# Kernel optimization log

Hardware: AMD Instinct MI355X
Metric: run time of the kernel (lower is better)

The kernel has to match this reference:

```python
import jax, jax.numpy as jnp
import numpy as np

HEADS = 8
RADIUS = 50
EPS = 1e-5


def conv1d(x, w, b, stride, pad):
    # x: [B, Cin, T], w: [Cout, Cin, K] (torch OIH layout)
    y = jax.lax.conv_general_dilated(x, w, (stride,), [(pad, pad)],
                                     dimension_numbers=("NCH", "OIH", "NCH"))
    return y + b[None, :, None]


def mm1x1(x, w, b):
    # pointwise Conv1d: w [Cout, Cin]
    return jnp.einsum("oc,bct->bot", w, x) + b[None, :, None]


def lstm_layer(xT, Wih, Whh, bih, bhh):
    # xT: [T, B, Cin]; torch gate order i, f, g, o
    B = xT.shape[1]
    Hh = Whh.shape[1]
    h0 = jnp.zeros((B, Hh), xT.dtype)

    def step(carry, xt):
        h, c = carry
        g = xt @ Wih.T + h @ Whh.T + bih + bhh
        i, f, gg, o = jnp.split(g, 4, axis=-1)
        c = jax.nn.sigmoid(f) * c + jax.nn.sigmoid(i) * jnp.tanh(gg)
        h = jax.nn.sigmoid(o) * jnp.tanh(c)
        return (h, c), h

    _, ys = jax.lax.scan(step, (h0, h0), xT)
    return ys


def attention(x, q_w, q_b, k_w, k_b, c_w, c_b, rel_emb, fc_w, fc_b, bn_g, bn_b, attn_scale):
    B, C, L = x.shape
    D = C // HEADS
    split = lambda y: y.reshape(B, HEADS, D, L)
    q = split(mm1x1(x, q_w, q_b))
    k = split(mm1x1(x, k_w, k_b))
    cnt = split(mm1x1(x, c_w, c_b))
    dots = jnp.einsum("bhct,bhcs->bhts", q, k)  # no 1/sqrt(d): faithful to source
    steps = jnp.arange(L)
    rel = steps[:, None] - steps[None, :]                       # [L, L]
    embs = rel_emb[RADIUS + jnp.clip(rel, -RADIUS, RADIUS)]     # [L, L, D]
    dots = dots + 0.3 * jnp.einsum("bhct,tsc->bhts", q, embs)
    dots = jnp.where((jnp.abs(rel) <= RADIUS)[None, None], dots, -jnp.inf)
    w = jax.nn.softmax(dots, axis=-1)
    out = jnp.einsum("bhts,bhcs->bhct", w, cnt) + 0.3 * jnp.einsum("bhts,tsc->bhct", w, embs)
    out = out.reshape(B, C, L)
    out = mm1x1(out, fc_w, fc_b)
    # BatchNorm1d, training-mode statistics over (batch, time)
    mu = out.mean(axis=(0, 2), keepdims=True)
    var = ((out - mu) ** 2).mean(axis=(0, 2), keepdims=True)
    out = (out - mu) * jax.lax.rsqrt(var + EPS) * bn_g[None, :, None] + bn_b[None, :, None]
    return jax.nn.relu(out) * attn_scale[None, :, None]


def forward(meg, conv1_w, conv1_b, conv2_w, conv2_b, subj_emb,
            W_ih0, W_hh0, b_ih0, b_hh0, W_ih1, W_hh1, b_ih1, b_hh1,
            q_w, q_b, k_w, k_b, c_w, c_b, rel_emb, fc_w, fc_b, bn_g, bn_b,
            attn_scale, out_w, out_b, subjects):
    # ConvSequence encoder: two strided convs, LeakyReLU(0.0) == ReLU
    x = jax.nn.relu(conv1d(meg, conv1_w, conv1_b, 2, 2))
    x = jax.nn.relu(conv1d(x, conv2_w, conv2_b, 2, 2))          # [B, 512, L]
    B, _, L = x.shape
    emb = subj_emb[subjects]                                    # ScaledEmbedding, scale=1.0
    x = jnp.concatenate([x, jnp.broadcast_to(emb[:, :, None], (B, emb.shape[1], L))], axis=1)
    xT = x.transpose(2, 0, 1)                                   # [L, B, 576]
    xT = lstm_layer(xT, W_ih0, W_hh0, b_ih0, b_hh0)
    xT = lstm_layer(xT, W_ih1, W_hh1, b_ih1, b_hh1)
    x = xT.transpose(1, 2, 0)                                   # [B, 512, L]
    x = x + attention(x, q_w, q_b, k_w, k_b, c_w, c_b, rel_emb, fc_w, fc_b, bn_g, bn_b, attn_scale)
    return mm1x1(x, out_w, out_b)                               # [B, 128, L]


def setup_inputs() -> dict:
    key = jax.random.key(0)
    ks = iter(jax.random.split(key, 40))
    nk = lambda: next(ks)
    r = lambda shape, s=0.05: jax.random.normal(nk(), shape, jnp.float32) * s
    # relative-position embedding with the cumsum/sqrt init from the source
    rel = jax.random.normal(nk(), (2 * RADIUS + 1, 64), jnp.float32) * 0.05
    rel = jnp.cumsum(rel, axis=0) / jnp.sqrt(jnp.arange(1, 2 * RADIUS + 2, dtype=jnp.float32))[:, None]
    return dict(
        meg=jax.random.normal(nk(), (8, 273, 2048), jnp.float32),
        conv1_w=r((512, 273, 4)), conv1_b=r((512,)),
        conv2_w=r((512, 512, 4)), conv2_b=r((512,)),
        subj_emb=r((200, 64), 0.1),
        W_ih0=r((2048, 576)), W_hh0=r((2048, 512)), b_ih0=r((2048,)), b_hh0=r((2048,)),
        W_ih1=r((2048, 512)), W_hh1=r((2048, 512)), b_ih1=r((2048,)), b_hh1=r((2048,)),
        q_w=r((512, 512)), q_b=r((512,)),
        k_w=r((512, 512)), k_b=r((512,)),
        c_w=r((512, 512)), c_b=r((512,)),
        rel_emb=rel,
        fc_w=r((512, 512)), fc_b=r((512,)),
        bn_g=jnp.ones((512,), jnp.float32), bn_b=jnp.zeros((512,), jnp.float32),
        attn_scale=jnp.full((512,), 0.1, jnp.float32),
        out_w=r((128, 512)), out_b=r((128,)),
        subjects=jax.random.randint(nk(), (8,), 0, 200),
    )


def reference(meg, conv1_w, conv1_b, conv2_w, conv2_b, subj_emb,
              W_ih0, W_hh0, b_ih0, b_hh0, W_ih1, W_hh1, b_ih1, b_hh1,
              q_w, q_b, k_w, k_b, c_w, c_b, rel_emb, fc_w, fc_b, bn_g, bn_b,
              attn_scale, out_w, out_b, subjects):
    return forward(meg, conv1_w, conv1_b, conv2_w, conv2_b, subj_emb,
                   W_ih0, W_hh0, b_ih0, b_hh0, W_ih1, W_hh1, b_ih1, b_hh1,
                   q_w, q_b, k_w, k_b, c_w, c_b, rel_emb, fc_w, fc_b, bn_g, bn_b,
                   attn_scale, out_w, out_b, subjects)
```

## Files before the change

### kernel.cpp

```cpp
#include <hip/hip_runtime.h>
#include <cstdint>
#include <cmath>

typedef unsigned short u16;
typedef unsigned int u32;
typedef __attribute__((ext_vector_type(8))) short bf16x8;
typedef __attribute__((ext_vector_type(4))) float f32x4;

#define B_    8
#define T_IN  2048
#define CIN1  273
#define L1_   1025
#define L_    513
#define C_    512
#define CE_   576
#define M1_   (B_*L1_)
#define M_    (B_*L_)
#define K1_   (CIN1*4)
#define H_    8
#define D_    64
#define R_    50

__device__ __forceinline__ u32 f2bf_rne(float f) {
    u32 x = __float_as_uint(f);
    return (x + 0x7fffu + ((x >> 16) & 1u)) >> 16;
}

__device__ __forceinline__ u32 a_pair(const void* A, int m, int k, int lda, int amode, int Ksz) {
    if (amode == 2) {
        if (k >= K1_) return 0;
        int b = m / L1_, t = m - b * L1_;
        int ci = k >> 2, kk = k & 3;
        int it = 2 * t - 2 + kk;
        const float* mg = (const float*)A + ((size_t)(b * CIN1 + ci)) * T_IN;
        u32 lo = ((unsigned)it < (unsigned)T_IN)       ? f2bf_rne(mg[it])     : 0;
        u32 hi = ((unsigned)(it + 1) < (unsigned)T_IN) ? f2bf_rne(mg[it + 1]) : 0;
        return lo | (hi << 16);
    } else if (amode == 5) {
        int b = m / L_, t = m - b * L_;
        int kk = k >> 9, ci = k & 511;
        int it = 2 * t - 2 + kk;
        if ((unsigned)it >= (unsigned)L1_) return 0;
        return *(const u32*)((const u16*)A + ((size_t)(b * L1_ + it)) * 512 + ci);
    } else {
        return *(const u32*)((const u16*)A + (size_t)m * lda + k);
    }
}

__global__ __launch_bounds__(256) void gemm_kernel(
    const void* __restrict__ Aptr, const u32* __restrict__ Bp,
    const float* __restrict__ bias1, const float* __restrict__ bias2,
    float* __restrict__ Cf, u16* __restrict__ Cb,
    int Msz, int Nsz, int Ksz, int lda, int ldc, int amode, int cmode, int relu)
{
    __shared__ u16 As[64][40];
    __shared__ u16 Bs[64][40];

    int tid = threadIdx.x;
    int m0 = blockIdx.x * 64, n0 = blockIdx.y * 64;
    int wv = tid >> 6, lane = tid & 63;
    int lm = lane & 15, quad = lane >> 4;
    int kp = tid & 15, rw = tid >> 4;
    int Kh = Ksz >> 1;

    f32x4 acc[4];
#pragma unroll
    for (int nt = 0; nt < 4; ++nt)
#pragma unroll
        for (int r = 0; r < 4; ++r) acc[nt][r] = 0.f;

    for (int k0 = 0; k0 < Ksz; k0 += 32) {
        int pidx = (k0 >> 1) + kp;
#pragma unroll
        for (int i = 0; i < 4; ++i) {
            int row = rw + 16 * i;
            int k = k0 + 2 * kp;
            int m = m0 + row;
            u32 aw = 0;
            if (m < Msz && k < Ksz) aw = a_pair(Aptr, m, k, lda, amode, Ksz);
            *(u32*)&As[row][2 * kp] = aw;
            u32 bw = 0;
            if (pidx < Kh) bw = Bp[(size_t)(n0 + row) * Kh + pidx];
            *(u32*)&Bs[row][2 * kp] = bw;
        }
        __syncthreads();

        bf16x8 af = *(const bf16x8*)&As[wv * 16 + lm][quad * 8];
#pragma unroll
        for (int nt = 0; nt < 4; ++nt) {
            bf16x8 bf = *(const bf16x8*)&Bs[nt * 16 + lm][quad * 8];
            acc[nt] = __builtin_amdgcn_mfma_f32_16x16x32_bf16(af, bf, acc[nt], 0, 0, 0);
        }
        __syncthreads();
    }

#pragma unroll
    for (int nt = 0; nt < 4; ++nt) {
#pragma unroll
        for (int r = 0; r < 4; ++r) {
            int m = m0 + wv * 16 + quad * 4 + r;
            if (m >= Msz) continue;
            int n = n0 + nt * 16 + lm;
            float v = acc[nt][r] + bias1[n] + (bias2 ? bias2[n] : 0.f);
            if (relu) v = fmaxf(v, 0.f);
            if (cmode == 0) {
                Cf[(size_t)m * ldc + n] = v;
            } else if (cmode == 1) {
                int b = m / L_, t = m - b * L_;
                Cf[((size_t)(b * 128 + n)) * L_ + t] = v;
            } else if (cmode == 2) {
                int b = m / L_, t = m - b * L_;
                Cf[((size_t)(t * 8 + b)) * ldc + n] = v;
            } else {
                Cb[(size_t)m * ldc + n] = (u16)f2bf_rne(v);
            }
        }
    }
}

__global__ __launch_bounds__(256) void gemm_qkv(
    const u16* __restrict__ h1b,
    const u32* __restrict__ qwp, const u32* __restrict__ kwp, const u32* __restrict__ cwp,
    const float* __restrict__ qb, const float* __restrict__ kb, const float* __restrict__ cb,
    float* __restrict__ qo, float* __restrict__ ko, float* __restrict__ co)
{
    __shared__ u16 As[64][40];
    __shared__ u16 Bs[64][40];

    int tid = threadIdx.x;
    int which = blockIdx.y >> 3;
    int m0 = blockIdx.x * 64, n0 = (blockIdx.y & 7) * 64;
    const u32* Bp = which == 0 ? qwp : (which == 1 ? kwp : cwp);
    const float* bias = which == 0 ? qb : (which == 1 ? kb : cb);
    float* Cf = which == 0 ? qo : (which == 1 ? ko : co);

    int wv = tid >> 6, lane = tid & 63;
    int lm = lane & 15, quad = lane >> 4;
    int kp = tid & 15, rw = tid >> 4;

    f32x4 acc[4];
#pragma unroll
    for (int nt = 0; nt < 4; ++nt)
#pragma unroll
        for (int r = 0; r < 4; ++r) acc[nt][r] = 0.f;

    for (int k0 = 0; k0 < 512; k0 += 32) {
#pragma unroll
        for (int i = 0; i < 4; ++i) {
            int row = rw + 16 * i;
            int k = k0 + 2 * kp;
            int m = m0 + row;
            u32 aw = 0;
            if (m < M_) {
                int b = m / L_, t = m - b * L_;
                aw = *(const u32*)(h1b + ((size_t)(t * 8 + b)) * 512 + k);
            }
            *(u32*)&As[row][2 * kp] = aw;
            *(u32*)&Bs[row][2 * kp] = Bp[(size_t)(n0 + row) * 256 + (k0 >> 1) + kp];
        }
        __syncthreads();

        bf16x8 af = *(const bf16x8*)&As[wv * 16 + lm][quad * 8];
#pragma unroll
        for (int nt = 0; nt < 4; ++nt) {
            bf16x8 bf = *(const bf16x8*)&Bs[nt * 16 + lm][quad * 8];
            acc[nt] = __builtin_amdgcn_mfma_f32_16x16x32_bf16(af, bf, acc[nt], 0, 0, 0);
        }
        __syncthreads();
    }

#pragma unroll
    for (int nt = 0; nt < 4; ++nt) {
#pragma unroll
        for (int r = 0; r < 4; ++r) {
            int m = m0 + wv * 16 + quad * 4 + r;
            if (m >= M_) continue;
            int n = n0 + nt * 16 + lm;
            Cf[(size_t)m * 512 + n] = acc[nt][r] + bias[n];
        }
    }
}

__global__ __launch_bounds__(256) void emb_kernel(const float* __restrict__ semb,
                                                  const int* __restrict__ subj,
                                                  u16* __restrict__ x2b)
{
    int idx = blockIdx.x * 256 + threadIdx.x;
    if (idx >= M_ * 64) return;
    int m = idx >> 6, e = idx & 63;
    int b = m / L_;
    x2b[(size_t)m * CE_ + 512 + e] = (u16)f2bf_rne(semb[subj[b] * 64 + e]);
}

__global__ __launch_bounds__(256) void pack_b(const float* __restrict__ W, u32* __restrict__ P,
                                              int N, int K)
{
    int gid = blockIdx.x * 256 + threadIdx.x;
    int Kh = K >> 1;
    if (gid >= N * Kh) return;
    int n = gid / Kh, p = gid - n * Kh;
    int k = 2 * p;
    u32 lo = f2bf_rne(W[(size_t)n * K + k]);
    u32 hi = f2bf_rne(W[(size_t)n * K + k + 1]);
    P[gid] = lo | (hi << 16);
}

__global__ __launch_bounds__(256) void pack_post(const float* __restrict__ qw,
                                                 const float* __restrict__ kw,
                                                 const float* __restrict__ cw,
                                                 const float* __restrict__ fcw,
                                                 const float* __restrict__ outw,
                                                 u32* __restrict__ P)
{
    int gid = blockIdx.x * 256 + threadIdx.x;
    if (gid >= 557056) return;
    const float* W;
    int local;
    if (gid < 524288) {
        int wsel = gid >> 17;
        W = wsel == 0 ? qw : (wsel == 1 ? kw : (wsel == 2 ? cw : fcw));
        local = gid & 131071;
    } else {
        W = outw;
        local = gid - 524288;
    }
    int n = local >> 8, p = local & 255;
    int k = 2 * p;
    u32 lo = f2bf_rne(W[(size_t)n * 512 + k]);
    u32 hi = f2bf_rne(W[(size_t)n * 512 + k + 1]);
    P[gid] = lo | (hi << 16);
}

__global__ __launch_bounds__(256) void pack_w2k(const float* __restrict__ W, u32* __restrict__ P)
{
    int gid = blockIdx.x * 256 + threadIdx.x;
    int n = gid >> 10, p = gid & 1023;
    int kk = p >> 8, ci = (2 * p) & 511;
    u32 lo = f2bf_rne(W[(size_t)n * 2048 + ci * 4 + kk]);
    u32 hi = f2bf_rne(W[(size_t)n * 2048 + ci * 4 + 4 + kk]);
    P[gid] = lo | (hi << 16);
}

__global__ __launch_bounds__(256) void pack_w3(const float* __restrict__ W0,
                                               const float* __restrict__ W1,
                                               const float* __restrict__ W2,
                                               u32* __restrict__ P)
{
    int gid3 = blockIdx.x * 256 + threadIdx.x;
    int src = gid3 >> 19;
    int gid = gid3 & 524287;
    const float* W = src == 0 ? W0 : (src == 1 ? W1 : W2);
    int r = gid & 1, lane = (gid >> 1) & 63, i2 = (gid >> 7) & 1;
    int g = (gid >> 8) & 3, j = gid >> 10;
    int row = g * 512 + j;
    int c0 = 4 * (lane + 64 * i2) + 2 * r;
    u32 lo = f2bf_rne(W[(size_t)row * 512 + c0]);
    u32 hi = f2bf_rne(W[(size_t)row * 512 + c0 + 1]);
    P[gid3] = lo | (hi << 16);
}

__global__ __launch_bounds__(256, 1) void lstm_persist(
    const float* __restrict__ pre0,
    const u32* __restrict__ P0,
    const u32* __restrict__ P1,
    const u32* __restrict__ P2,
    const float* __restrict__ bih1,
    const float* __restrict__ bhh1,
    float* __restrict__ h0seq,
    float* __restrict__ h1seq,
    u16* __restrict__ h1b,
    u32* __restrict__ f0,
    u32* __restrict__ f1)
{
    const int layer = blockIdx.x >> 7;
    const int blk = blockIdx.x & 127;
    const int tid = threadIdx.x;
    const int l = tid & 63;
    const int rg = tid >> 6;
    const int j = blk * 4 + rg;

    __shared__ float4 hA4[1024];
    __shared__ float4 hB4[1024];
    __shared__ float part[4 * 8 * 33];
    __shared__ float gates[4 * 33];

    const u32* wA = (layer ? P2 : P0) + (size_t)j * 1024;
    uint2 wra[8], wrb[8];
#pragma unroll
    for (int i2 = 0; i2 < 2; ++i2)
#pragma unroll
        for (int g = 0; g < 4; ++g)
            wra[i2 * 4 + g] = *(const uint2*)&wA[(g * 2 + i2) * 128 + l * 2];
    if (layer) {
        const u32* wB = P1 + (size_t)j * 1024;
#pragma unroll
        for (int i2 = 0; i2 < 2; ++i2)
#pragma unroll
            for (int g = 0; g < 4; ++g)
                wrb[i2 * 4 + g] = *(const uint2*)&wB[(g * 2 + i2) * 128 + l * 2];
    }

    int fb = 0, grow = 0;
    float bias1 = 0.f;
    if (tid < 128) {
        int fw = tid >> 5;
        fb = tid & 7;
        grow = ((tid & 31) >> 3) * 512 + blk * 4 + fw;
        if (layer) bias1 = bih1[grow] + bhh1[grow];
    }

    float creg = 0.f;

    for (int t = 0; t <= L_; ++t) {
        bool active = layer ? (t >= 1) : (t < L_);
        if (!active) continue;
        int tt = layer ? (t - 1) : t;

        float mypre = 0.f;
        if (tid < 128)
            mypre = layer ? bias1 : pre0[((size_t)(tt * 8 + fb)) * 2048 + grow];

        if (tid < 64) {
            const u32* sA = nullptr;
            const u32* sB = nullptr;
            if (layer) {
                sA = f0 + (size_t)tt * 128;
                if (tt > 0) sB = f1 + (size_t)(tt - 1) * 128;
            } else if (tt > 0) {
                sA = f0 + (size_t)(tt - 1) * 128;
            }
            if (sA) {
                bool a0 = false, a1 = false;
                bool b0 = (sB == nullptr), b1 = (sB == nullptr);
                for (;;) {
                    if (!a0) a0 = __hip_atomic_load(&sA[l], __ATOMIC_RELAXED, __HIP_MEMORY_SCOPE_AGENT) != 0u;
                    if (!a1) a1 = __hip_atomic_load(&sA[l + 64], __ATOMIC_RELAXED, __HIP_MEMORY_SCOPE_AGENT) != 0u;
                    if (sB) {
                        if (!b0) b0 = __hip_atomic_load(&sB[l], __ATOMIC_RELAXED, __HIP_MEMORY_SCOPE_AGENT) != 0u;
                        if (!b1) b1 = __hip_atomic_load(&sB[l + 64], __ATOMIC_RELAXED, __HIP_MEMORY_SCOPE_AGENT) != 0u;
                    }
                    if (__all(a0 && a1 && b0 && b1)) break;
                    __builtin_amdgcn_s_sleep(1);
                }
            }
        }
        __syncthreads();

        if (tt == 0) {
#pragma unroll
            for (int i = 0; i < 4; ++i)
                hA4[tid + 256 * i] = make_float4(0.f, 0.f, 0.f, 0.f);
        } else {
            const float4* src = (const float4*)((layer ? h1seq : h0seq) + (size_t)(tt - 1) * 4096);
#pragma unroll
            for (int i = 0; i < 4; ++i)
                hA4[tid + 256 * i] = src[tid + 256 * i];
        }
        if (layer) {
            const float4* src = (const float4*)(h0seq + (size_t)tt * 4096);
#pragma unroll
            for (int i = 0; i < 4; ++i)
                hB4[tid + 256 * i] = src[tid + 256 * i];
        }
        __syncthreads();

        float acc[4][8];
#pragma unroll
        for (int g = 0; g < 4; ++g)
#pragma unroll
            for (int b = 0; b < 8; ++b) acc[g][b] = 0.f;

#pragma unroll
        for (int i2 = 0; i2 < 2; ++i2) {
            int cq = l + 64 * i2;
            float4 hv[8];
#pragma unroll
            for (int b = 0; b < 8; ++b) hv[b] = hA4[b * 128 + cq];
#pragma unroll
            for (int g = 0; g < 4; ++g) {
                uint2 ww = wra[i2 * 4 + g];
                float w0 = __uint_as_float(ww.x << 16);
                float w1 = __uint_as_float(ww.x & 0xffff0000u);
                float w2 = __uint_as_float(ww.y << 16);
                float w3 = __uint_as_float(ww.y & 0xffff0000u);
#pragma unroll
                for (int b = 0; b < 8; ++b)
                    acc[g][b] = fmaf(w0, hv[b].x, fmaf(w1, hv[b].y,
                                fmaf(w2, hv[b].z, fmaf(w3, hv[b].w, acc[g][b]))));
            }
        }
        if (layer) {
#pragma unroll
            for (int i2 = 0; i2 < 2; ++i2) {
                int cq = l + 64 * i2;
                float4 hv[8];
#pragma unroll
                for (int b = 0; b < 8; ++b) hv[b] = hB4[b * 128 + cq];
#pragma unroll
                for (int g = 0; g < 4; ++g) {
                    uint2 ww = wrb[i2 * 4 + g];
                    float w0 = __uint_as_float(ww.x << 16);
                    float w1 = __uint_as_float(ww.x & 0xffff0000u);
                    float w2 = __uint_as_float(ww.y << 16);
                    float w3 = __uint_as_float(ww.y & 0xffff0000u);
#pragma unroll
                    for (int b = 0; b < 8; ++b)
                        acc[g][b] = fmaf(w0, hv[b].x, fmaf(w1, hv[b].y,
                                    fmaf(w2, hv[b].z, fmaf(w3, hv[b].w, acc[g][b]))));
                }
            }
        }

#pragma unroll
        for (int m = 8; m <= 32; m <<= 1)
#pragma unroll
            for (int g = 0; g < 4; ++g)
#pragma unroll
                for (int b = 0; b < 8; ++b)
                    acc[g][b] += __shfl_xor(acc[g][b], m);
        if (l < 8) {
#pragma unroll
            for (int g = 0; g < 4; ++g)
#pragma unroll
                for (int b = 0; b < 8; ++b)
                    part[(rg * 8 + l) * 33 + g * 8 + b] = acc[g][b];
        }
        __syncthreads();

        if (tid < 128) {
            int w = tid >> 5, x = tid & 31;
            float s = 0.f;
#pragma unroll
            for (int p = 0; p < 8; ++p) s += part[(w * 8 + p) * 33 + x];
            gates[w * 33 + x] = s + mypre;
        }
        __syncthreads();

        if (tid < 32) {
            int w = tid >> 3, b = tid & 7;
            float gi = gates[w * 33 + 0 * 8 + b];
            float gf = gates[w * 33 + 1 * 8 + b];
            float gg = gates[w * 33 + 2 * 8 + b];
            float go = gates[w * 33 + 3 * 8 + b];
            int ji = blk * 4 + w;
            float cprev = (tt == 0) ? 0.f : creg;
            float si = 1.f / (1.f + expf(-gi));
            float sf = 1.f / (1.f + expf(-gf));
            float so = 1.f / (1.f + expf(-go));
            float cn = sf * cprev + si * tanhf(gg);
            creg = cn;
            float hv = so * tanhf(cn);
            float* hout = layer ? h1seq : h0seq;
            __hip_atomic_store(&hout[((size_t)tt * 8 + b) * 512 + ji], hv,
                               __ATOMIC_RELAXED, __HIP_MEMORY_SCOPE_AGENT);
            if (layer) h1b[((size_t)tt * 8 + b) * 512 + ji] = (u16)f2bf_rne(hv);
        }
        asm volatile("s_waitcnt vmcnt(0)" ::: "memory");
        if (tid == 0)
            __hip_atomic_store((layer ? f1 : f0) + (size_t)tt * 128 + blk, 1u,
                               __ATOMIC_RELAXED, __HIP_MEMORY_SCOPE_AGENT);
        __syncthreads();
    }
}

__global__ __launch_bounds__(128) void attn_kernel(const float* __restrict__ q,
                                                   const float* __restrict__ k,
                                                   const float* __restrict__ cnt,
                                                   const float* __restrict__ rel,
                                                   u16* __restrict__ outb)
{
    int t = blockIdx.x, h = blockIdx.y, b = blockIdx.z;
    int s_lo = max(0, t - R_), s_hi = min(L_ - 1, t + R_);
    int W = s_hi - s_lo + 1;
    int tid = threadIdx.x;

    __shared__ float qrow[64];
    __shared__ float dots[104];
    __shared__ float red[128];

    const float* qp = q + ((size_t)(b * L_ + t) * C_ + h * D_);
    if (tid < 64) qrow[tid] = qp[tid];
    __syncthreads();

    if (tid < W) {
        int s = s_lo + tid;
        const float* kp = k + ((size_t)(b * L_ + s) * C_ + h * D_);
        const float* rp = rel + (R_ + t - s) * D_;
        float acc = 0.f;
#pragma unroll 8
        for (int d = 0; d < 64; ++d)
            acc += qrow[d] * (kp[d] + 0.3f * rp[d]);
        dots[tid] = acc;
    }
    __syncthreads();

    red[tid] = (tid < W) ? dots[tid] : -INFINITY;
    __syncthreads();
    for (int s = 64; s > 0; s >>= 1) {
        if (tid < s) red[tid] = fmaxf(red[tid], red[tid + s]);
        __syncthreads();
    }
    float mx = red[0];
    __syncthreads();
    float e = 0.f;
    if (tid < W) { e = expf(dots[tid] - mx); dots[tid] = e; }
    red[tid] = e;
    __syncthreads();
    for (int s = 64; s > 0; s >>= 1) {
        if (tid < s) red[tid] += red[tid + s];
        __syncthreads();
    }
    float inv = 1.f / red[0];
    if (tid < W) dots[tid] *= inv;
    __syncthreads();

    if (tid < 64) {
        float acc = 0.f;
        const float* cb = cnt + ((size_t)(b * L_ + s_lo) * C_ + h * D_ + tid);
        const float* rb = rel + (R_ + t - s_lo) * D_ + tid;
        for (int i = 0; i < W; ++i)
            acc += dots[i] * (cb[(size_t)i * C_] + 0.3f * rb[-i * D_]);
        outb[(size_t)(b * L_ + t) * C_ + h * D_ + tid] = (u16)f2bf_rne(acc);
    }
}

__global__ __launch_bounds__(512) void bn_sum(const float* __restrict__ fcout, float* __restrict__ stats)
{
    int c = threadIdx.x;
    float s = 0.f, ss = 0.f;
    for (int m = blockIdx.x; m < M_; m += 32) {
        float v = fcout[(size_t)m * 512 + c];
        s += v; ss += v * v;
    }
    atomicAdd(&stats[c], s);
    atomicAdd(&stats[512 + c], ss);
}

__global__ __launch_bounds__(256) void bn_apply(const float* __restrict__ fcout,
                                                const float* __restrict__ stats,
                                                const float* __restrict__ bng, const float* __restrict__ bnb,
                                                const float* __restrict__ ascl,
                                                const float* __restrict__ h1tm,
                                                u16* __restrict__ xfinb)
{
    int idx = blockIdx.x * 256 + threadIdx.x;
    if (idx >= M_ * 512) return;
    int c = idx & 511;
    int m = idx >> 9;
    int b = m / L_, t = m - b * L_;
    float mean = stats[c] * (1.f / (float)M_);
    float var = stats[512 + c] * (1.f / (float)M_) - mean * mean;
    float rs = rsqrtf(fmaxf(var, 0.f) + 1e-5f);
    float v = (fcout[idx] - mean) * rs * bng[c] + bnb[c];
    v = fmaxf(v, 0.f) * ascl[c];
    xfinb[idx] = (u16)f2bf_rne(h1tm[((size_t)(t * 8 + b)) * 512 + c] + v);
}

extern "C" void kernel_launch(void* const* d_in, const int* in_sizes, int n_in,
                              void* d_out, int out_size, void* d_ws, size_t ws_size,
                              hipStream_t stream)
{
    const float* meg  = (const float*)d_in[0];
    const float* w1   = (const float*)d_in[1];
    const float* b1   = (const float*)d_in[2];
    const float* w2   = (const float*)d_in[3];
    const float* b2   = (const float*)d_in[4];
    const float* semb = (const float*)d_in[5];
    const float* Wih0 = (const float*)d_in[6];
    const float* Whh0 = (const float*)d_in[7];
    const float* bih0 = (const float*)d_in[8];
    const float* bhh0 = (const float*)d_in[9];
    const float* Wih1 = (const float*)d_in[10];
    const float* Whh1 = (const float*)d_in[11];
    const float* bih1 = (const float*)d_in[12];
    const float* bhh1 = (const float*)d_in[13];
    const float* qw   = (const float*)d_in[14];
    const float* qb   = (const float*)d_in[15];
    const float* kw   = (const float*)d_in[16];
    const float* kb   = (const float*)d_in[17];
    const float* cw   = (const float*)d_in[18];
    const float* cbi  = (const float*)d_in[19];
    const float* rel  = (const float*)d_in[20];
    const float* fcw  = (const float*)d_in[21];
    const float* fcb  = (const float*)d_in[22];
    const float* bng  = (const float*)d_in[23];
    const float* bnb  = (const float*)d_in[24];
    const float* ascl = (const float*)d_in[25];
    const float* outw = (const float*)d_in[26];
    const float* outb = (const float*)d_in[27];
    const int* subj = (const int*)d_in[28];
    float* out = (float*)d_out;

    float* ws = (float*)d_ws;
    u16*   x1b   = (u16*)(ws + 0);
    u32*   w1p   = (u32*)(ws + 6562304);
    u32*   w2p   = (u32*)(ws + 6841856);
    u16*   x2b   = (u16*)(ws + 4198400);
    u32*   wih0p = (u32*)(ws + 14967296);
    u32*   P0    = (u32*)(ws + 0);
    u32*   P1    = (u32*)(ws + 524288);
    u32*   P2    = (u32*)(ws + 1048576);
    u32*   flg   = (u32*)(ws + 1572864);
    float* pre0  = ws + 6562304;
    float* h0    = ws + 14967296;
    float* h1    = ws + 17068544;
    u16*   h1b   = (u16*)(ws + 19169792);
    float* qb_f  = ws + 0;
    float* kb_f  = ws + 2101248;
    float* cb_f  = ws + 4202496;
    u16*   attno = (u16*)(ws + 6562304);
    float* fco   = ws + 8663552;
    float* stats = ws + 10764800;
    u32*   qwp   = (u32*)(ws + 10765824);
    u32*   kwp   = (u32*)(ws + 10896896);
    u32*   cwp   = (u32*)(ws + 11027968);
    u32*   fcwp  = (u32*)(ws + 11159040);
    u32*   outwp = (u32*)(ws + 11290112);
    u16*   xfinb = (u16*)(ws + 19169792);

    auto gemm = [&](const void* A, const u32* Bp, const float* bi1, const float* bi2,
                    float* Cf, u16* Cb, int Msz, int Nsz, int Ksz,
                    int lda, int ldc, int amode, int cmode, int relu) {
        dim3 g((Msz + 63) / 64, Nsz / 64);
        gemm_kernel<<<g, 256, 0, stream>>>(A, Bp, bi1, bi2, Cf, Cb,
                                           Msz, Nsz, Ksz, lda, ldc, amode, cmode, relu);
    };

    pack_b<<<(512 * 546 + 255) / 256, 256, 0, stream>>>(w1, w1p, 512, 1092);
    pack_w2k<<<2048, 256, 0, stream>>>(w2, w2p);

    gemm(meg, w1p, b1, nullptr, nullptr, x1b, M1_, 512, K1_, 0, 512, 2, 3, 1);
    gemm(x1b, w2p, b2, nullptr, nullptr, x2b, M_, 512, 2048, 0, CE_, 5, 3, 1);
    emb_kernel<<<(M_ * 64 + 255) / 256, 256, 0, stream>>>(semb, subj, x2b);

    pack_w3<<<6144, 256, 0, stream>>>(Whh0, Wih1, Whh1, P0);
    pack_b<<<(2048 * 288 + 255) / 256, 256, 0, stream>>>(Wih0, wih0p, 2048, 576);

    gemm(x2b, wih0p, bih0, bhh0, pre0, nullptr, M_, 2048, CE_, CE_, 2048, 6, 2, 0);

    hipMemsetAsync(flg, 0, 2 * 514 * 128 * sizeof(u32), stream);
    lstm_persist<<<dim3(256), 256, 0, stream>>>(pre0, P0, P1, P2, bih1, bhh1,
                                                h0, h1, h1b, flg, flg + 514 * 128);

    pack_post<<<(557056 + 255) / 256, 256, 0, stream>>>(qw, kw, cw, fcw, outw, qwp);
    hipMemsetAsync(stats, 0, 1024 * sizeof(float), stream);

    gemm_qkv<<<dim3((M_ + 63) / 64, 24), 256, 0, stream>>>(h1b, qwp, kwp, cwp, qb, kb, cbi,
                                                           qb_f, kb_f, cb_f);

    attn_kernel<<<dim3(L_, H_, B_), 128, 0, stream>>>(qb_f, kb_f, cb_f, rel, attno);

    gemm(attno, fcwp, fcb, nullptr, fco, nullptr, M_, 512, 512, 512, 512, 6, 0, 0);
    bn_sum<<<32, 512, 0, stream>>>(fco, stats);
    bn_apply<<<(M_ * 512 + 255) / 256, 256, 0, stream>>>(fco, stats, bng, bnb, ascl, h1, xfinb);

    gemm(xfinb, outwp, outb, nullptr, out, nullptr, M_, 128, 512, 512, 0, 6, 1, 0);
}
```

Before: 3.691 ms.

## Drop LDS staging of hidden state in persistent LSTM, read h directly per wave

Each wave of the persistent LSTM kernel now polls the cross-block readiness flags itself. It then loads the previous hidden state straight from global memory into registers, instead of one wave polling and the block staging h into shared memory. This removes two block-wide barriers per timestep plus the trailing barrier, and moves the bf16 copy of h1 after the flag publish so it is off the critical path. The latency-bound recurrence should advance faster per step. In exchange each of the four waves re-reads the full hidden vector from L2, and memory ordering now relies more on per-wave flag polling.

```diff
diff --git a/kernel.cpp b/kernel.cpp
--- a/kernel.cpp
+++ b/kernel.cpp
@@ -279,8 +279,6 @@
     const int rg = tid >> 6;
     const int j = blk * 4 + rg;
 
-    __shared__ float4 hA4[1024];
-    __shared__ float4 hB4[1024];
     __shared__ float part[4 * 8 * 33];
     __shared__ float gates[4 * 33];
 
@@ -310,6 +308,7 @@
     }
 
     float creg = 0.f;
+    const float4 z4 = make_float4(0.f, 0.f, 0.f, 0.f);
 
     for (int t = 0; t <= L_; ++t) {
         bool active = layer ? (t >= 1) : (t < L_);
@@ -320,7 +319,7 @@
         if (tid < 128)
             mypre = layer ? bias1 : pre0[((size_t)(tt * 8 + fb)) * 2048 + grow];
 
-        if (tid < 64) {
+        {
             const u32* sA = nullptr;
             const u32* sB = nullptr;
             if (layer) {
@@ -344,25 +343,7 @@
                 }
             }
         }
-        __syncthreads();
-
-        if (tt == 0) {
-#pragma unroll
-            for (int i = 0; i < 4; ++i)
-                hA4[tid + 256 * i] = make_float4(0.f, 0.f, 0.f, 0.f);
-        } else {
-            const float4* src = (const float4*)((layer ? h1seq : h0seq) + (size_t)(tt - 1) * 4096);
-#pragma unroll
-            for (int i = 0; i < 4; ++i)
-                hA4[tid + 256 * i] = src[tid + 256 * i];
-        }
-        if (layer) {
-            const float4* src = (const float4*)(h0seq + (size_t)tt * 4096);
-#pragma unroll
-            for (int i = 0; i < 4; ++i)
-                hB4[tid + 256 * i] = src[tid + 256 * i];
-        }
-        __syncthreads();
+        asm volatile("" ::: "memory");
 
         float acc[4][8];
 #pragma unroll
@@ -370,12 +351,19 @@
 #pragma unroll
             for (int b = 0; b < 8; ++b) acc[g][b] = 0.f;
 
+        const float* hsrcA = layer ? h1seq : h0seq;
 #pragma unroll
         for (int i2 = 0; i2 < 2; ++i2) {
             int cq = l + 64 * i2;
             float4 hv[8];
-#pragma unroll
-            for (int b = 0; b < 8; ++b) hv[b] = hA4[b * 128 + cq];
+            if (tt > 0) {
+                const float4* hp = (const float4*)(hsrcA + (size_t)(tt - 1) * 4096);
+#pragma unroll
+                for (int b = 0; b < 8; ++b) hv[b] = hp[b * 128 + cq];
+            } else {
+#pragma unroll
+                for (int b = 0; b < 8; ++b) hv[b] = z4;
+            }
 #pragma unroll
             for (int g = 0; g < 4; ++g) {
                 uint2 ww = wra[i2 * 4 + g];
@@ -390,12 +378,13 @@
             }
         }
         if (layer) {
+            const float4* gp = (const float4*)(h0seq + (size_t)tt * 4096);
 #pragma unroll
             for (int i2 = 0; i2 < 2; ++i2) {
                 int cq = l + 64 * i2;
                 float4 hv[8];
 #pragma unroll
-                for (int b = 0; b < 8; ++b) hv[b] = hB4[b * 128 + cq];
+                for (int b = 0; b < 8; ++b) hv[b] = gp[b * 128 + cq];
 #pragma unroll
                 for (int g = 0; g < 4; ++g) {
                     uint2 ww = wrb[i2 * 4 + g];
@@ -436,6 +425,7 @@
         }
         __syncthreads();
 
+        float hstore = 0.f;
         if (tid < 32) {
             int w = tid >> 3, b = tid & 7;
             float gi = gates[w * 33 + 0 * 8 + b];
@@ -449,17 +439,19 @@
             float so = 1.f / (1.f + expf(-go));
             float cn = sf * cprev + si * tanhf(gg);
             creg = cn;
-            float hv = so * tanhf(cn);
+            hstore = so * tanhf(cn);
             float* hout = layer ? h1seq : h0seq;
-            __hip_atomic_store(&hout[((size_t)tt * 8 + b) * 512 + ji], hv,
+            __hip_atomic_store(&hout[((size_t)(tt * 8 + b)) * 512 + ji], hstore,
                                __ATOMIC_RELAXED, __HIP_MEMORY_SCOPE_AGENT);
-            if (layer) h1b[((size_t)tt * 8 + b) * 512 + ji] = (u16)f2bf_rne(hv);
-        }
-        asm volatile("s_waitcnt vmcnt(0)" ::: "memory");
+        }
+        if (rg == 0) { asm volatile("s_waitcnt vmcnt(0)" ::: "memory"); }
         if (tid == 0)
             __hip_atomic_store((layer ? f1 : f0) + (size_t)tt * 128 + blk, 1u,
                                __ATOMIC_RELAXED, __HIP_MEMORY_SCOPE_AGENT);
-        __syncthreads();
+        if (layer && tid < 32) {
+            int w = tid >> 3, b = tid & 7;
+            h1b[((size_t)(tt * 8 + b)) * 512 + blk * 4 + w] = (u16)f2bf_rne(hstore);
+        }
     }
 }
 
```

Result: slower. 5.066 ms (+37.2%).
